# Optimization experiments

Measured on AMD Instinct MI355X. Metric: run time of the kernel, lower is better.

## Reference

```python
import jax, jax.numpy as jnp
import numpy as np

B, S, E, H, NQ, FF = 4, 1024, 256, 32, 8, 1024
DK = E // H  # 8, equals n_wires of the quantum attention layer
EPS = 1e-5


def layernorm(x, g, b):
    mu = jnp.mean(x, axis=-1, keepdims=True)
    var = jnp.mean(jnp.square(x - mu), axis=-1, keepdims=True)
    return (x - mu) * jax.lax.rsqrt(var + EPS) * g + b


def setup_inputs() -> dict:
    key = jax.random.key(0)
    ks = jax.random.split(key, 20)
    s = lambda n: 1.0 / np.sqrt(n)
    return {
        "x": jax.random.normal(ks[0], (B, S, E), dtype=jnp.float32),
        # quantum attention trainable RX angles (one per wire)
        "theta_attn": jax.random.uniform(ks[1], (DK,), minval=-np.pi, maxval=np.pi),
        # nn.MultiheadAttention packed in-proj and out-proj
        "w_in": jax.random.normal(ks[2], (3 * E, E)) * s(E),
        "b_in": jnp.zeros((3 * E,), jnp.float32),
        "w_out": jax.random.normal(ks[3], (E, E)) * s(E),
        "b_out": jnp.zeros((E,), jnp.float32),
        # combine linear
        "w_comb": jax.random.normal(ks[4], (E, E)) * s(E),
        "b_comb": jnp.zeros((E,), jnp.float32),
        # layernorms
        "g1": jnp.ones((E,), jnp.float32), "be1": jnp.zeros((E,), jnp.float32),
        "g2": jnp.ones((E,), jnp.float32), "be2": jnp.zeros((E,), jnp.float32),
        # FFN: input_proj, quantum RY angles, linear1, linear2
        "w_ip": jax.random.normal(ks[5], (NQ, E)) * s(E),
        "b_ip": jnp.zeros((NQ,), jnp.float32),
        "theta_ffn": jax.random.uniform(ks[6], (NQ,), minval=-np.pi, maxval=np.pi),
        "w1": jax.random.normal(ks[7], (FF, NQ)) * s(NQ),
        "b1": jnp.zeros((FF,), jnp.float32),
        "w2": jax.random.normal(ks[8], (E, FF)) * s(FF),
        "b2": jnp.zeros((E,), jnp.float32),
    }


def reference(x, theta_attn, w_in, b_in, w_out, b_out, w_comb, b_comb,
              g1, be1, g2, be2, w_ip, b_ip, theta_ffn, w1, b1, w2, b2):
    batch, seq, embed = x.shape
    # ---- QuantumAttention ----
    # per-head RX(x_i) encoding followed by trainable RX(theta_i): <Z_i> = cos(x_i + theta_i)
    xh = x.reshape(batch, seq, H, DK)            # [B,S,H,dk]
    q_out = jnp.cos(xh + theta_attn).reshape(batch, seq, embed)
    # standard multi-head self-attention on q_out (q=k=v)
    qkv = q_out @ w_in.T + b_in                  # [B,S,3E]
    q, k, v = jnp.split(qkv, 3, axis=-1)
    def heads(t):
        return t.reshape(batch, seq, H, DK).transpose(0, 2, 1, 3)  # [B,H,S,dk]
    q, k, v = heads(q), heads(k), heads(v)
    scores = jnp.einsum('bhqd,bhkd->bhqk', q, k) / np.sqrt(DK)
    attn = jax.nn.softmax(scores, axis=-1)
    ctx = jnp.einsum('bhqk,bhkd->bhqd', attn, v)
    ctx = ctx.transpose(0, 2, 1, 3).reshape(batch, seq, embed)
    attn_out = (ctx @ w_out.T + b_out) @ w_comb.T + b_comb
    # ---- residual + norm1 ----
    h = layernorm(x + attn_out, g1, be1)
    # ---- QuantumFeedForward ----
    proj = h @ w_ip.T + b_ip                     # [B,S,NQ]
    # RX(x) encoding then trainable RY(phi): <Z> = cos(phi) * cos(x)
    qf = jnp.cos(theta_ffn) * jnp.cos(proj)
    ffn_out = jax.nn.relu(qf @ w1.T + b1) @ w2.T + b2
    # ---- residual + norm2 ----
    return layernorm(h + ffn_out, g2, be2)
```

## Files before the change

kernel.cpp:

```cpp
#include <hip/hip_runtime.h>
#include <hip/hip_bf16.h>

#define B_  4
#define S_  1024
#define E_  256
#define H_  32
#define NQ_ 8
#define FF_ 1024
#define M_  (B_*S_)
#define QS  0.5100880289202462f
#define VSTRIDE 1036

typedef __attribute__((ext_vector_type(8))) short bf16x8;
typedef __attribute__((ext_vector_type(4))) short short4v;
typedef __attribute__((ext_vector_type(4))) float f32x4;

#if __has_builtin(__builtin_amdgcn_exp2f)
#define EXP2 __builtin_amdgcn_exp2f
#else
#define EXP2 exp2f
#endif

__device__ inline short f2bf(float f) {
    union { float f; unsigned u; } v; v.f = f;
    unsigned r = (v.u + 0x7fff + ((v.u >> 16) & 1)) >> 16;
    return (short)r;
}

__device__ inline float bf2f(ushort u_) {
    union { unsigned u; float f; } c; c.u = ((unsigned)u_) << 16; return c.f;
}

__device__ inline unsigned pk2(float a, float b) {
    __hip_bfloat162 h = __float22bfloat162_rn(make_float2(a, b));
    union { __hip_bfloat162 h; unsigned u; } c; c.h = h;
    return c.u;
}

__global__ __launch_bounds__(256) void d1_kernel(
        const float* __restrict__ x, const float* __restrict__ theta_attn,
        const float* __restrict__ w_in, const float* __restrict__ b_in,
        const float* __restrict__ w_out, const float* __restrict__ w_comb,
        const float* __restrict__ b_out, const float* __restrict__ b_comb,
        const float* __restrict__ w2,
        ushort* __restrict__ qkv_bf, ushort* __restrict__ weff_bf,
        float* __restrict__ beff, ushort* __restrict__ w2_bf) {
    __shared__ ushort As[128 * 64];
    __shared__ ushort Bs[64 * 64];
    __shared__ float red[4];
    int bid = blockIdx.x, tid = threadIdx.x;

    if (bid >= 392) {
        if (bid < 648) {
            int i = bid - 392;
            float p = w_comb[(size_t)i * 256 + tid] * b_out[tid];
#pragma unroll
            for (int o = 32; o > 0; o >>= 1) p += __shfl_xor(p, o);
            if ((tid & 63) == 0) red[tid >> 6] = p;
            __syncthreads();
            if (tid == 0) beff[i] = red[0] + red[1] + red[2] + red[3] + b_comb[i];
        } else {
            int i = (bid - 648) * 256 + tid;
            float4 v = ((const float4*)w2)[i];
            short4v o = {f2bf(v.x), f2bf(v.y), f2bf(v.z), f2bf(v.w)};
            ((short4v*)w2_bf)[i] = o;
        }
        return;
    }

    bool isW = bid >= 384;
    int bm, bn;
    if (!isW) { bm = (bid / 12) * 128; bn = (bid % 12) * 64; }
    else      { int t = bid - 384; bm = (t >> 2) * 128; bn = (t & 3) * 64; }

    int w = tid >> 6, l = tid & 63, lq = l & 15, hi = l >> 4;
    int wm = w & 1, wn = w >> 1;
    f32x4 acc[4][2] = {};
    int srow = tid >> 3;
    int sk = (tid & 7) * 8;
    float wscale = isW ? 1.f : ((bn < 256) ? QS : 1.f);
    float th[8];
    if (!isW) {
#pragma unroll
        for (int j = 0; j < 8; ++j) th[j] = theta_attn[j];
    }

    for (int k0 = 0; k0 < 256; k0 += 64) {
        __syncthreads();
        if (!isW) {
#pragma unroll
            for (int it = 0; it < 4; ++it) {
                int row = it * 32 + srow;
                const float* xp = x + (size_t)(bm + row) * 256 + k0 + sk;
                float4 a = *(const float4*)xp;
                float4 b = *(const float4*)(xp + 4);
                bf16x8 o;
                o[0] = f2bf(__cosf(a.x + th[0]));
                o[1] = f2bf(__cosf(a.y + th[1]));
                o[2] = f2bf(__cosf(a.z + th[2]));
                o[3] = f2bf(__cosf(a.w + th[3]));
                o[4] = f2bf(__cosf(b.x + th[4]));
                o[5] = f2bf(__cosf(b.y + th[5]));
                o[6] = f2bf(__cosf(b.z + th[6]));
                o[7] = f2bf(__cosf(b.w + th[7]));
                *(bf16x8*)((char*)As + row * 128 + ((sk * 2) ^ ((row & 7) << 4))) = o;
            }
#pragma unroll
            for (int it = 0; it < 2; ++it) {
                int row = it * 32 + srow;
                const float* wp = w_in + (size_t)(bn + row) * 256 + k0 + sk;
                float4 a = *(const float4*)wp;
                float4 b = *(const float4*)(wp + 4);
                bf16x8 o;
                o[0] = f2bf(a.x * wscale); o[1] = f2bf(a.y * wscale);
                o[2] = f2bf(a.z * wscale); o[3] = f2bf(a.w * wscale);
                o[4] = f2bf(b.x * wscale); o[5] = f2bf(b.y * wscale);
                o[6] = f2bf(b.z * wscale); o[7] = f2bf(b.w * wscale);
                *(bf16x8*)((char*)Bs + row * 128 + ((sk * 2) ^ ((row & 7) << 4))) = o;
            }
        } else {
#pragma unroll
            for (int it = 0; it < 4; ++it) {
                int row = it * 32 + srow;
                const float* wp = w_comb + (size_t)(bm + row) * 256 + k0 + sk;
                float4 a = *(const float4*)wp;
                float4 b = *(const float4*)(wp + 4);
                bf16x8 o;
                o[0] = f2bf(a.x); o[1] = f2bf(a.y); o[2] = f2bf(a.z); o[3] = f2bf(a.w);
                o[4] = f2bf(b.x); o[5] = f2bf(b.y); o[6] = f2bf(b.z); o[7] = f2bf(b.w);
                *(bf16x8*)((char*)As + row * 128 + ((sk * 2) ^ ((row & 7) << 4))) = o;
            }
            int nl = tid & 63, kg = tid >> 6;
#pragma unroll
            for (int kk = 0; kk < 16; ++kk) {
                int kb = (kg * 16 + kk) * 2;
                float v = w_out[(size_t)(k0 + kg * 16 + kk) * 256 + bn + nl];
                *(ushort*)((char*)Bs + nl * 128 + (kb ^ ((nl & 7) << 4))) = (ushort)f2bf(v);
            }
        }
        __syncthreads();
#pragma unroll
        for (int kk = 0; kk < 2; ++kk) {
            bf16x8 af[4], bfr[2];
#pragma unroll
            for (int mf = 0; mf < 4; ++mf) {
                int row = wm * 64 + mf * 16 + lq;
                af[mf] = *(const bf16x8*)((const char*)As + row * 128 +
                                          ((kk * 64 + hi * 16) ^ ((row & 7) << 4)));
            }
#pragma unroll
            for (int nf = 0; nf < 2; ++nf) {
                int row = wn * 32 + nf * 16 + lq;
                bfr[nf] = *(const bf16x8*)((const char*)Bs + row * 128 +
                                           ((kk * 64 + hi * 16) ^ ((row & 7) << 4)));
            }
#pragma unroll
            for (int mf = 0; mf < 4; ++mf)
#pragma unroll
                for (int nf = 0; nf < 2; ++nf)
                    acc[mf][nf] = __builtin_amdgcn_mfma_f32_16x16x32_bf16(af[mf], bfr[nf], acc[mf][nf], 0, 0, 0);
        }
    }
    ushort* Cp = isW ? weff_bf : qkv_bf;
    int Nd = isW ? 256 : 768;
#pragma unroll
    for (int mf = 0; mf < 4; ++mf)
#pragma unroll
        for (int nf = 0; nf < 2; ++nf) {
            int n = bn + wn * 32 + nf * 16 + lq;
            float bv = isW ? 0.f : b_in[n] * wscale;
#pragma unroll
            for (int r = 0; r < 4; ++r) {
                int m = bm + wm * 64 + mf * 16 + hi * 4 + r;
                Cp[(size_t)m * Nd + n] = (ushort)f2bf(acc[mf][nf][r] + bv);
            }
        }
}

__global__ __launch_bounds__(256, 4) void attn_mfma_kernel(const ushort* __restrict__ qkv,
                                                           ushort* __restrict__ ctx) {
    __shared__ ushort ks[S_ * 8];
    __shared__ ushort vt[9 * VSTRIDE + 4];
    int qt = blockIdx.x, h = blockIdx.y, b = blockIdx.z;
    int tid = threadIdx.x;
    const ushort* base = qkv + (size_t)b * S_ * (3 * E_) + h * 8;

    for (int i = tid; i < S_; i += 256) {
        const ushort* rp = base + (size_t)i * (3 * E_);
        bf16x8 kv = *(const bf16x8*)(rp + E_);
        bf16x8 vv = *(const bf16x8*)(rp + 2 * E_);
        *(bf16x8*)&ks[i * 8] = kv;
        int kf = (i >> 4) & 3, hh = (i >> 2) & 3, s = i & 3;
        int pv = (i & ~63) + ((kf >> 1) << 5) + (hh << 3) + ((kf & 1) << 2) + s;
#pragma unroll
        for (int d = 0; d < 8; ++d) vt[d * VSTRIDE + pv] = vv[d];
        vt[8 * VSTRIDE + pv] = 0x3F80;
    }
    __syncthreads();

    int w = tid >> 6, l = tid & 63, lq = l & 15, g = l >> 4;

    bf16x8 qfrag[2];
#pragma unroll
    for (int qf = 0; qf < 2; ++qf) {
        bf16x8 qv = {};
        if (g == 0)
            qv = *(const bf16x8*)(base + (size_t)(qt * 128 + w * 32 + qf * 16 + lq) * (3 * E_));
        qfrag[qf] = qv;
    }

    f32x4 ctxa[2] = {{0.f,0.f,0.f,0.f},{0.f,0.f,0.f,0.f}};
    const f32x4 zf = {0.f, 0.f, 0.f, 0.f};

    for (int kt = 0; kt < 16; ++kt) {
        bf16x8 kfrag[4];
#pragma unroll
        for (int kf = 0; kf < 4; ++kf) {
            bf16x8 kv = {};
            if (g == 0) kv = *(bf16x8*)&ks[(kt * 64 + kf * 16 + lq) * 8];
            kfrag[kf] = kv;
        }
        bf16x8 vf0 = *(bf16x8*)&vt[lq * VSTRIDE + kt * 64 + g * 8];
        bf16x8 vf1 = *(bf16x8*)&vt[lq * VSTRIDE + kt * 64 + 32 + g * 8];
#pragma unroll
        for (int qf = 0; qf < 2; ++qf) {
            f32x4 st[4];
#pragma unroll
            for (int kf = 0; kf < 4; ++kf)
                st[kf] = __builtin_amdgcn_mfma_f32_16x16x32_bf16(kfrag[kf], qfrag[qf], zf, 0, 0, 0);
            union { unsigned u[4]; bf16x8 v; } p0, p1;
            p0.u[0] = pk2(EXP2(st[0][0]), EXP2(st[0][1]));
            p0.u[1] = pk2(EXP2(st[0][2]), EXP2(st[0][3]));
            p0.u[2] = pk2(EXP2(st[1][0]), EXP2(st[1][1]));
            p0.u[3] = pk2(EXP2(st[1][2]), EXP2(st[1][3]));
            p1.u[0] = pk2(EXP2(st[2][0]), EXP2(st[2][1]));
            p1.u[1] = pk2(EXP2(st[2][2]), EXP2(st[2][3]));
            p1.u[2] = pk2(EXP2(st[3][0]), EXP2(st[3][1]));
            p1.u[3] = pk2(EXP2(st[3][2]), EXP2(st[3][3]));
            ctxa[qf] = __builtin_amdgcn_mfma_f32_16x16x32_bf16(p0.v, vf0, ctxa[qf], 0, 0, 0);
            ctxa[qf] = __builtin_amdgcn_mfma_f32_16x16x32_bf16(p1.v, vf1, ctxa[qf], 0, 0, 0);
        }
    }

#pragma unroll
    for (int qf = 0; qf < 2; ++qf) {
        int src = (l & 48) + 8;
        float s0 = __shfl(ctxa[qf][0], src);
        float s1 = __shfl(ctxa[qf][1], src);
        float s2 = __shfl(ctxa[qf][2], src);
        float s3 = __shfl(ctxa[qf][3], src);
        if (lq < 8) {
            int tok = b * S_ + qt * 128 + w * 32 + qf * 16 + g * 4;
            ushort* cp = ctx + (size_t)tok * E_ + h * 8 + lq;
            cp[0]      = (ushort)f2bf(ctxa[qf][0] / s0);
            cp[E_]     = (ushort)f2bf(ctxa[qf][1] / s1);
            cp[2 * E_] = (ushort)f2bf(ctxa[qf][2] / s2);
            cp[3 * E_] = (ushort)f2bf(ctxa[qf][3] / s3);
        }
    }
}

__global__ __launch_bounds__(256) void d3_kernel(
        const ushort* __restrict__ ctx, const ushort* __restrict__ weff,
        const float* __restrict__ beff, const float* __restrict__ x,
        const float* __restrict__ g1, const float* __restrict__ be1,
        const float* __restrict__ w_ip, const float* __restrict__ b_ip,
        const float* __restrict__ theta_ffn,
        float* __restrict__ h, float* __restrict__ qf) {
    __shared__ union {
        struct { ushort As[16 * 64]; ushort Bs[256 * 64]; } st;
        ushort hl[16 * 264];
    } u;
    __shared__ float red[2][16][4];
    int tid = threadIdx.x;
    int bm = blockIdx.x * 16;
    int wn = tid >> 6, l = tid & 63, lq = l & 15, hi = l >> 4;
    f32x4 acc[4] = {};

    for (int k0 = 0; k0 < 256; k0 += 64) {
        __syncthreads();
        if (tid < 128) {
            int row = tid >> 3, sk = (tid & 7) * 8;
            bf16x8 v = *(const bf16x8*)(ctx + (size_t)(bm + row) * 256 + k0 + sk);
            *(bf16x8*)((char*)u.st.As + row * 128 + ((sk * 2) ^ ((row & 7) << 4))) = v;
        }
#pragma unroll
        for (int it = 0; it < 8; ++it) {
            int v8 = it * 256 + tid;
            int row = v8 >> 3, kb = (v8 & 7) * 16;
            bf16x8 v = *(const bf16x8*)(weff + (size_t)row * 256 + k0 + (kb >> 1));
            *(bf16x8*)((char*)u.st.Bs + row * 128 + (kb ^ ((row & 7) << 4))) = v;
        }
        __syncthreads();
#pragma unroll
        for (int kk = 0; kk < 2; ++kk) {
            bf16x8 af, bfr[4];
            af = *(const bf16x8*)((const char*)u.st.As + lq * 128 +
                                  ((kk * 64 + hi * 16) ^ ((lq & 7) << 4)));
#pragma unroll
            for (int nf = 0; nf < 4; ++nf) {
                int row = wn * 64 + nf * 16 + lq;
                bfr[nf] = *(const bf16x8*)((const char*)u.st.Bs + row * 128 +
                                           ((kk * 64 + hi * 16) ^ ((row & 7) << 4)));
            }
#pragma unroll
            for (int nf = 0; nf < 4; ++nf)
                acc[nf] = __builtin_amdgcn_mfma_f32_16x16x32_bf16(af, bfr[nf], acc[nf], 0, 0, 0);
        }
    }
    __syncthreads();

    float vv[4][4];
    float rs[4] = {}, rq[4] = {};
#pragma unroll
    for (int nf = 0; nf < 4; ++nf) {
        int n = wn * 64 + nf * 16 + lq;
        float bv = beff[n];
#pragma unroll
        for (int r = 0; r < 4; ++r) {
            int m = bm + hi * 4 + r;
            float val = acc[nf][r] + bv + x[(size_t)m * 256 + n];
            vv[nf][r] = val;
            rs[r] += val;
            rq[r] += val * val;
        }
    }
#pragma unroll
    for (int o = 1; o < 16; o <<= 1)
#pragma unroll
        for (int r = 0; r < 4; ++r) {
            rs[r] += __shfl_xor(rs[r], o);
            rq[r] += __shfl_xor(rq[r], o);
        }
    if (lq == 0) {
#pragma unroll
        for (int r = 0; r < 4; ++r) {
            red[0][hi * 4 + r][wn] = rs[r];
            red[1][hi * 4 + r][wn] = rq[r];
        }
    }
    __syncthreads();
#pragma unroll
    for (int r = 0; r < 4; ++r) {
        int row = hi * 4 + r;
        float st_ = red[0][row][0] + red[0][row][1] + red[0][row][2] + red[0][row][3];
        float sq_ = red[1][row][0] + red[1][row][1] + red[1][row][2] + red[1][row][3];
        float mu = st_ * (1.f / 256.f);
        float var = sq_ * (1.f / 256.f) - mu * mu;
        rs[r] = mu;
        rq[r] = rsqrtf(var + 1e-5f);
    }
    __syncthreads();
#pragma unroll
    for (int nf = 0; nf < 4; ++nf) {
        int n = wn * 64 + nf * 16 + lq;
        float gn = g1[n], bn_ = be1[n];
#pragma unroll
        for (int r = 0; r < 4; ++r) {
            int row = hi * 4 + r;
            float vn = (vv[nf][r] - rs[r]) * rq[r] * gn + bn_;
            h[(size_t)(bm + row) * 256 + n] = vn;
            u.hl[row * 264 + n] = (ushort)f2bf(vn);
        }
    }
    __syncthreads();

    if (tid < 128) {
        int tok = tid >> 3, wq = tid & 7;
        const float* wip = w_ip + wq * 256;
        float pr = 0.f;
#pragma unroll
        for (int c = 0; c < 32; ++c) {
            bf16x8 hv = *(const bf16x8*)&u.hl[tok * 264 + c * 8];
            float4 wa = *(const float4*)(wip + c * 8);
            float4 wb = *(const float4*)(wip + c * 8 + 4);
            pr += bf2f((ushort)hv[0]) * wa.x + bf2f((ushort)hv[1]) * wa.y
                + bf2f((ushort)hv[2]) * wa.z + bf2f((ushort)hv[3]) * wa.w
                + bf2f((ushort)hv[4]) * wb.x + bf2f((ushort)hv[5]) * wb.y
                + bf2f((ushort)hv[6]) * wb.z + bf2f((ushort)hv[7]) * wb.w;
        }
        qf[(size_t)(bm + tok) * NQ_ + wq] = __cosf(theta_ffn[wq]) * __cosf(pr + b_ip[wq]);
    }
}

__global__ __launch_bounds__(256) void d4_kernel(
        const float* __restrict__ qf, const float* __restrict__ w1,
        const float* __restrict__ b1, const ushort* __restrict__ w2b,
        const float* __restrict__ b2, const float* __restrict__ h,
        const float* __restrict__ g2, const float* __restrict__ be2,
        float* __restrict__ out) {
    __shared__ ushort As[16 * 64];
    __shared__ ushort Bs[256 * 64];
    __shared__ ushort w1l[FF_ * 8];
    __shared__ float b1l[FF_];
    __shared__ float qfl[16 * 8];
    __shared__ float red[2][16][4];
    int tid = threadIdx.x;
    int bm = blockIdx.x * 16;
    int wn = tid >> 6, l = tid & 63, lq = l & 15, hi = l >> 4;
    f32x4 acc[4] = {};

#pragma unroll
    for (int it = 0; it < 32; ++it) w1l[it * 256 + tid] = (ushort)f2bf(w1[it * 256 + tid]);
#pragma unroll
    for (int it = 0; it < 4; ++it) b1l[it * 256 + tid] = b1[it * 256 + tid];
    if (tid < 128) qfl[tid] = qf[(size_t)bm * NQ_ + tid];
    __syncthreads();

    for (int k0 = 0; k0 < 1024; k0 += 64) {
        __syncthreads();
        if (tid < 128) {
            int row = tid >> 3, j8 = tid & 7;
            int f0 = k0 + j8 * 8;
            float q[8];
#pragma unroll
            for (int k = 0; k < 8; ++k) q[k] = qfl[row * 8 + k];
            bf16x8 o;
#pragma unroll
            for (int j = 0; j < 8; ++j) {
                bf16x8 wv = *(const bf16x8*)&w1l[(f0 + j) * 8];
                float s = b1l[f0 + j];
#pragma unroll
                for (int k = 0; k < 8; ++k) s += q[k] * bf2f((ushort)wv[k]);
                o[j] = f2bf(fmaxf(s, 0.f));
            }
            int sk = j8 * 8;
            *(bf16x8*)((char*)As + row * 128 + ((sk * 2) ^ ((row & 7) << 4))) = o;
        }
#pragma unroll
        for (int it = 0; it < 8; ++it) {
            int v8 = it * 256 + tid;
            int row = v8 >> 3, kb = (v8 & 7) * 16;
            bf16x8 v = *(const bf16x8*)(w2b + (size_t)row * 1024 + k0 + (kb >> 1));
            *(bf16x8*)((char*)Bs + row * 128 + (kb ^ ((row & 7) << 4))) = v;
        }
        __syncthreads();
#pragma unroll
        for (int kk = 0; kk < 2; ++kk) {
            bf16x8 af, bfr[4];
            af = *(const bf16x8*)((const char*)As + lq * 128 +
                                  ((kk * 64 + hi * 16) ^ ((lq & 7) << 4)));
#pragma unroll
            for (int nf = 0; nf < 4; ++nf) {
                int row = wn * 64 + nf * 16 + lq;
                bfr[nf] = *(const bf16x8*)((const char*)Bs + row * 128 +
                                           ((kk * 64 + hi * 16) ^ ((row & 7) << 4)));
            }
#pragma unroll
            for (int nf = 0; nf < 4; ++nf)
                acc[nf] = __builtin_amdgcn_mfma_f32_16x16x32_bf16(af, bfr[nf], acc[nf], 0, 0, 0);
        }
    }

    float vv[4][4];
    float rs[4] = {}, rq[4] = {};
#pragma unroll
    for (int nf = 0; nf < 4; ++nf) {
        int n = wn * 64 + nf * 16 + lq;
        float bv = b2[n];
#pragma unroll
        for (int r = 0; r < 4; ++r) {
            int m = bm + hi * 4 + r;
            float val = acc[nf][r] + bv + h[(size_t)m * 256 + n];
            vv[nf][r] = val;
            rs[r] += val;
            rq[r] += val * val;
        }
    }
#pragma unroll
    for (int o = 1; o < 16; o <<= 1)
#pragma unroll
        for (int r = 0; r < 4; ++r) {
            rs[r] += __shfl_xor(rs[r], o);
            rq[r] += __shfl_xor(rq[r], o);
        }
    if (lq == 0) {
#pragma unroll
        for (int r = 0; r < 4; ++r) {
            red[0][hi * 4 + r][wn] = rs[r];
            red[1][hi * 4 + r][wn] = rq[r];
        }
    }
    __syncthreads();
#pragma unroll
    for (int r = 0; r < 4; ++r) {
        int row = hi * 4 + r;
        float st_ = red[0][row][0] + red[0][row][1] + red[0][row][2] + red[0][row][3];
        float sq_ = red[1][row][0] + red[1][row][1] + red[1][row][2] + red[1][row][3];
        float mu = st_ * (1.f / 256.f);
        float var = sq_ * (1.f / 256.f) - mu * mu;
        rs[r] = mu;
        rq[r] = rsqrtf(var + 1e-5f);
    }
#pragma unroll
    for (int nf = 0; nf < 4; ++nf) {
        int n = wn * 64 + nf * 16 + lq;
        float gn = g2[n], bn_ = be2[n];
#pragma unroll
        for (int r = 0; r < 4; ++r) {
            int row = hi * 4 + r;
            out[(size_t)(bm + row) * 256 + n] =
                (vv[nf][r] - rs[r]) * rq[r] * gn + bn_;
        }
    }
}

extern "C" void kernel_launch(void* const* d_in, const int* in_sizes, int n_in,
                              void* d_out, int out_size, void* d_ws, size_t ws_size,
                              hipStream_t stream) {
    const float* x          = (const float*)d_in[0];
    const float* theta_attn = (const float*)d_in[1];
    const float* w_in       = (const float*)d_in[2];
    const float* b_in       = (const float*)d_in[3];
    const float* w_out      = (const float*)d_in[4];
    const float* b_out      = (const float*)d_in[5];
    const float* w_comb     = (const float*)d_in[6];
    const float* b_comb     = (const float*)d_in[7];
    const float* g1         = (const float*)d_in[8];
    const float* be1        = (const float*)d_in[9];
    const float* g2         = (const float*)d_in[10];
    const float* be2        = (const float*)d_in[11];
    const float* w_ip       = (const float*)d_in[12];
    const float* b_ip       = (const float*)d_in[13];
    const float* theta_ffn  = (const float*)d_in[14];
    const float* w1         = (const float*)d_in[15];
    const float* b1         = (const float*)d_in[16];
    const float* w2         = (const float*)d_in[17];
    const float* b2         = (const float*)d_in[18];
    float* out = (float*)d_out;

    char* wsb = (char*)d_ws;
    ushort* qkv_bf  = (ushort*)(wsb);
    ushort* ctx_bf  = (ushort*)(wsb + (6u << 20));
    float*  h       = (float*)(wsb + (8u << 20));
    float*  qf      = (float*)(wsb + (12u << 20));
    ushort* weff_bf = (ushort*)(wsb + (13u << 20));
    ushort* w2_bf   = (ushort*)(wsb + (13u << 20) + 131072);
    float*  beff    = (float*)(wsb + (14u << 20));

    d1_kernel<<<904, 256, 0, stream>>>(x, theta_attn, w_in, b_in, w_out, w_comb,
                                       b_out, b_comb, w2, qkv_bf, weff_bf, beff, w2_bf);
    attn_mfma_kernel<<<dim3(S_ / 128, H_, B_), 256, 0, stream>>>(qkv_bf, ctx_bf);
    d3_kernel<<<M_ / 16, 256, 0, stream>>>(ctx_bf, weff_bf, beff, x, g1, be1,
                                           w_ip, b_ip, theta_ffn, h, qf);
    d4_kernel<<<M_ / 16, 256, 0, stream>>>(qf, w1, b1, w2_bf, b2, h, g2, be2, out);
}
```

Baseline: 183.0 us.

## Fuse norm1/FFN kernels and read GEMM operands directly from global

Merges the d3 and d4 kernels into one, so h and qf stay in shared memory instead of round-tripping through global workspace, and removes one launch. The FFN hidden activations (relu(qf@w1^T+b1)) are computed once into a full 16x1024 LDS tile, and both GEMMs now load weight fragments straight from global/L2 instead of staging them through LDS with barriers. The attention inner loop also raises wave priority around the MFMA/exp section. In exchange, LDS use per block grows and the uncoalesced direct global fragment loads may lose bandwidth efficiency. The FFN projection now uses fp32 h instead of bf16.

Result: no change. 183.0 us (-0.0%).

```diff
diff --git a/kernel.cpp b/kernel.cpp
--- a/kernel.cpp
+++ b/kernel.cpp
@@ -222,6 +222,7 @@
         }
         bf16x8 vf0 = *(bf16x8*)&vt[lq * VSTRIDE + kt * 64 + g * 8];
         bf16x8 vf1 = *(bf16x8*)&vt[lq * VSTRIDE + kt * 64 + 32 + g * 8];
+        __builtin_amdgcn_s_setprio(1);
 #pragma unroll
         for (int qf = 0; qf < 2; ++qf) {
             f32x4 st[4];
@@ -240,6 +241,7 @@
             ctxa[qf] = __builtin_amdgcn_mfma_f32_16x16x32_bf16(p0.v, vf0, ctxa[qf], 0, 0, 0);
             ctxa[qf] = __builtin_amdgcn_mfma_f32_16x16x32_bf16(p1.v, vf1, ctxa[qf], 0, 0, 0);
         }
+        __builtin_amdgcn_s_setprio(0);
     }
 
 #pragma unroll
@@ -260,55 +262,38 @@
     }
 }
 
-__global__ __launch_bounds__(256) void d3_kernel(
+__global__ __launch_bounds__(256) void d34_kernel(
         const ushort* __restrict__ ctx, const ushort* __restrict__ weff,
         const float* __restrict__ beff, const float* __restrict__ x,
         const float* __restrict__ g1, const float* __restrict__ be1,
         const float* __restrict__ w_ip, const float* __restrict__ b_ip,
         const float* __restrict__ theta_ffn,
-        float* __restrict__ h, float* __restrict__ qf) {
-    __shared__ union {
-        struct { ushort As[16 * 64]; ushort Bs[256 * 64]; } st;
-        ushort hl[16 * 264];
-    } u;
+        const float* __restrict__ w1, const float* __restrict__ b1,
+        const ushort* __restrict__ w2b, const float* __restrict__ b2,
+        const float* __restrict__ g2, const float* __restrict__ be2,
+        float* __restrict__ out) {
+    __shared__ float hs[16 * 260];
+    __shared__ float qfl[16 * 8];
+    __shared__ ushort ts[16 * 1024];
     __shared__ float red[2][16][4];
     int tid = threadIdx.x;
     int bm = blockIdx.x * 16;
     int wn = tid >> 6, l = tid & 63, lq = l & 15, hi = l >> 4;
+
     f32x4 acc[4] = {};
-
+#pragma unroll
     for (int k0 = 0; k0 < 256; k0 += 64) {
-        __syncthreads();
-        if (tid < 128) {
-            int row = tid >> 3, sk = (tid & 7) * 8;
-            bf16x8 v = *(const bf16x8*)(ctx + (size_t)(bm + row) * 256 + k0 + sk);
-            *(bf16x8*)((char*)u.st.As + row * 128 + ((sk * 2) ^ ((row & 7) << 4))) = v;
-        }
-#pragma unroll
-        for (int it = 0; it < 8; ++it) {
-            int v8 = it * 256 + tid;
-            int row = v8 >> 3, kb = (v8 & 7) * 16;
-            bf16x8 v = *(const bf16x8*)(weff + (size_t)row * 256 + k0 + (kb >> 1));
-            *(bf16x8*)((char*)u.st.Bs + row * 128 + (kb ^ ((row & 7) << 4))) = v;
-        }
-        __syncthreads();
 #pragma unroll
         for (int kk = 0; kk < 2; ++kk) {
-            bf16x8 af, bfr[4];
-            af = *(const bf16x8*)((const char*)u.st.As + lq * 128 +
-                                  ((kk * 64 + hi * 16) ^ ((lq & 7) << 4)));
+            bf16x8 af = *(const bf16x8*)(ctx + (size_t)(bm + lq) * 256 + k0 + kk * 32 + hi * 8);
 #pragma unroll
             for (int nf = 0; nf < 4; ++nf) {
-                int row = wn * 64 + nf * 16 + lq;
-                bfr[nf] = *(const bf16x8*)((const char*)u.st.Bs + row * 128 +
-                                           ((kk * 64 + hi * 16) ^ ((row & 7) << 4)));
-            }
-#pragma unroll
-            for (int nf = 0; nf < 4; ++nf)
-                acc[nf] = __builtin_amdgcn_mfma_f32_16x16x32_bf16(af, bfr[nf], acc[nf], 0, 0, 0);
-        }
-    }
-    __syncthreads();
+                int rb = wn * 64 + nf * 16 + lq;
+                bf16x8 bf_ = *(const bf16x8*)(weff + (size_t)rb * 256 + k0 + kk * 32 + hi * 8);
+                acc[nf] = __builtin_amdgcn_mfma_f32_16x16x32_bf16(af, bf_, acc[nf], 0, 0, 0);
+            }
+        }
+    }
 
     float vv[4][4];
     float rs[4] = {}, rq[4] = {};
@@ -350,7 +335,6 @@
         rs[r] = mu;
         rq[r] = rsqrtf(var + 1e-5f);
     }
-    __syncthreads();
 #pragma unroll
     for (int nf = 0; nf < 4; ++nf) {
         int n = wn * 64 + nf * 16 + lq;
@@ -358,9 +342,7 @@
 #pragma unroll
         for (int r = 0; r < 4; ++r) {
             int row = hi * 4 + r;
-            float vn = (vv[nf][r] - rs[r]) * rq[r] * gn + bn_;
-            h[(size_t)(bm + row) * 256 + n] = vn;
-            u.hl[row * 264 + n] = (ushort)f2bf(vn);
+            hs[row * 260 + n] = (vv[nf][r] - rs[r]) * rq[r] * gn + bn_;
         }
     }
     __syncthreads();
@@ -370,115 +352,82 @@
         const float* wip = w_ip + wq * 256;
         float pr = 0.f;
 #pragma unroll
-        for (int c = 0; c < 32; ++c) {
-            bf16x8 hv = *(const bf16x8*)&u.hl[tok * 264 + c * 8];
-            float4 wa = *(const float4*)(wip + c * 8);
-            float4 wb = *(const float4*)(wip + c * 8 + 4);
-            pr += bf2f((ushort)hv[0]) * wa.x + bf2f((ushort)hv[1]) * wa.y
-                + bf2f((ushort)hv[2]) * wa.z + bf2f((ushort)hv[3]) * wa.w
-                + bf2f((ushort)hv[4]) * wb.x + bf2f((ushort)hv[5]) * wb.y
-                + bf2f((ushort)hv[6]) * wb.z + bf2f((ushort)hv[7]) * wb.w;
-        }
-        qf[(size_t)(bm + tok) * NQ_ + wq] = __cosf(theta_ffn[wq]) * __cosf(pr + b_ip[wq]);
-    }
-}
-
-__global__ __launch_bounds__(256) void d4_kernel(
-        const float* __restrict__ qf, const float* __restrict__ w1,
-        const float* __restrict__ b1, const ushort* __restrict__ w2b,
-        const float* __restrict__ b2, const float* __restrict__ h,
-        const float* __restrict__ g2, const float* __restrict__ be2,
-        float* __restrict__ out) {
-    __shared__ ushort As[16 * 64];
-    __shared__ ushort Bs[256 * 64];
-    __shared__ ushort w1l[FF_ * 8];
-    __shared__ float b1l[FF_];
-    __shared__ float qfl[16 * 8];
-    __shared__ float red[2][16][4];
-    int tid = threadIdx.x;
-    int bm = blockIdx.x * 16;
-    int wn = tid >> 6, l = tid & 63, lq = l & 15, hi = l >> 4;
-    f32x4 acc[4] = {};
-
-#pragma unroll
-    for (int it = 0; it < 32; ++it) w1l[it * 256 + tid] = (ushort)f2bf(w1[it * 256 + tid]);
-#pragma unroll
-    for (int it = 0; it < 4; ++it) b1l[it * 256 + tid] = b1[it * 256 + tid];
-    if (tid < 128) qfl[tid] = qf[(size_t)bm * NQ_ + tid];
-    __syncthreads();
-
+        for (int c = 0; c < 64; ++c) {
+            float4 hv = *(const float4*)&hs[tok * 260 + c * 4];
+            float4 wv = *(const float4*)(wip + c * 4);
+            pr += hv.x * wv.x + hv.y * wv.y + hv.z * wv.z + hv.w * wv.w;
+        }
+        qfl[tok * 8 + wq] = __cosf(theta_ffn[wq]) * __cosf(pr + b_ip[wq]);
+    }
+    __syncthreads();
+
+    {
+        int row = tid & 15, fb = tid >> 4;
+        float q[8];
+#pragma unroll
+        for (int k = 0; k < 8; ++k) q[k] = qfl[row * 8 + k];
+#pragma unroll
+        for (int j8 = 0; j8 < 8; ++j8) {
+            int f0 = fb * 64 + j8 * 8;
+            bf16x8 o;
+#pragma unroll
+            for (int j = 0; j < 8; ++j) {
+                const float* wp = w1 + (size_t)(f0 + j) * 8;
+                float4 wa = *(const float4*)wp;
+                float4 wb = *(const float4*)(wp + 4);
+                float s = b1[f0 + j]
+                        + q[0] * wa.x + q[1] * wa.y + q[2] * wa.z + q[3] * wa.w
+                        + q[4] * wb.x + q[5] * wb.y + q[6] * wb.z + q[7] * wb.w;
+                o[j] = f2bf(fmaxf(s, 0.f));
+            }
+            *(bf16x8*)((char*)ts + row * 2048 + ((f0 * 2) ^ ((row & 7) << 4))) = o;
+        }
+    }
+    __syncthreads();
+
+    f32x4 acc2[4] = {};
+#pragma unroll 4
     for (int k0 = 0; k0 < 1024; k0 += 64) {
-        __syncthreads();
-        if (tid < 128) {
-            int row = tid >> 3, j8 = tid & 7;
-            int f0 = k0 + j8 * 8;
-            float q[8];
-#pragma unroll
-            for (int k = 0; k < 8; ++k) q[k] = qfl[row * 8 + k];
-            bf16x8 o;
-#pragma unroll
-            for (int j = 0; j < 8; ++j) {
-                bf16x8 wv = *(const bf16x8*)&w1l[(f0 + j) * 8];
-                float s = b1l[f0 + j];
-#pragma unroll
-                for (int k = 0; k < 8; ++k) s += q[k] * bf2f((ushort)wv[k]);
-                o[j] = f2bf(fmaxf(s, 0.f));
-            }
-            int sk = j8 * 8;
-            *(bf16x8*)((char*)As + row * 128 + ((sk * 2) ^ ((row & 7) << 4))) = o;
-        }
-#pragma unroll
-        for (int it = 0; it < 8; ++it) {
-            int v8 = it * 256 + tid;
-            int row = v8 >> 3, kb = (v8 & 7) * 16;
-            bf16x8 v = *(const bf16x8*)(w2b + (size_t)row * 1024 + k0 + (kb >> 1));
-            *(bf16x8*)((char*)Bs + row * 128 + (kb ^ ((row & 7) << 4))) = v;
-        }
-        __syncthreads();
 #pragma unroll
         for (int kk = 0; kk < 2; ++kk) {
-            bf16x8 af, bfr[4];
-            af = *(const bf16x8*)((const char*)As + lq * 128 +
-                                  ((kk * 64 + hi * 16) ^ ((lq & 7) << 4)));
+            bf16x8 af = *(const bf16x8*)((const char*)ts + lq * 2048 +
+                                         ((k0 * 2 + kk * 64 + hi * 16) ^ ((lq & 7) << 4)));
 #pragma unroll
             for (int nf = 0; nf < 4; ++nf) {
-                int row = wn * 64 + nf * 16 + lq;
-                bfr[nf] = *(const bf16x8*)((const char*)Bs + row * 128 +
-                                           ((kk * 64 + hi * 16) ^ ((row & 7) << 4)));
-            }
-#pragma unroll
-            for (int nf = 0; nf < 4; ++nf)
-                acc[nf] = __builtin_amdgcn_mfma_f32_16x16x32_bf16(af, bfr[nf], acc[nf], 0, 0, 0);
-        }
-    }
-
-    float vv[4][4];
-    float rs[4] = {}, rq[4] = {};
+                int rb = wn * 64 + nf * 16 + lq;
+                bf16x8 bf_ = *(const bf16x8*)(w2b + (size_t)rb * 1024 + k0 + kk * 32 + hi * 8);
+                acc2[nf] = __builtin_amdgcn_mfma_f32_16x16x32_bf16(af, bf_, acc2[nf], 0, 0, 0);
+            }
+        }
+    }
+
+    float rs2[4] = {}, rq2[4] = {};
 #pragma unroll
     for (int nf = 0; nf < 4; ++nf) {
         int n = wn * 64 + nf * 16 + lq;
         float bv = b2[n];
 #pragma unroll
         for (int r = 0; r < 4; ++r) {
-            int m = bm + hi * 4 + r;
-            float val = acc[nf][r] + bv + h[(size_t)m * 256 + n];
+            int row = hi * 4 + r;
+            float val = acc2[nf][r] + bv + hs[row * 260 + n];
             vv[nf][r] = val;
-            rs[r] += val;
-            rq[r] += val * val;
+            rs2[r] += val;
+            rq2[r] += val * val;
         }
     }
 #pragma unroll
     for (int o = 1; o < 16; o <<= 1)
 #pragma unroll
         for (int r = 0; r < 4; ++r) {
-            rs[r] += __shfl_xor(rs[r], o);
-            rq[r] += __shfl_xor(rq[r], o);
-        }
+            rs2[r] += __shfl_xor(rs2[r], o);
+            rq2[r] += __shfl_xor(rq2[r], o);
+        }
+    __syncthreads();
     if (lq == 0) {
 #pragma unroll
         for (int r = 0; r < 4; ++r) {
-            red[0][hi * 4 + r][wn] = rs[r];
-            red[1][hi * 4 + r][wn] = rq[r];
+            red[0][hi * 4 + r][wn] = rs2[r];
+            red[1][hi * 4 + r][wn] = rq2[r];
         }
     }
     __syncthreads();
@@ -489,8 +438,8 @@
         float sq_ = red[1][row][0] + red[1][row][1] + red[1][row][2] + red[1][row][3];
         float mu = st_ * (1.f / 256.f);
         float var = sq_ * (1.f / 256.f) - mu * mu;
-        rs[r] = mu;
-        rq[r] = rsqrtf(var + 1e-5f);
+        rs2[r] = mu;
+        rq2[r] = rsqrtf(var + 1e-5f);
     }
 #pragma unroll
     for (int nf = 0; nf < 4; ++nf) {
@@ -500,7 +449,7 @@
         for (int r = 0; r < 4; ++r) {
             int row = hi * 4 + r;
             out[(size_t)(bm + row) * 256 + n] =
-                (vv[nf][r] - rs[r]) * rq[r] * gn + bn_;
+                (vv[nf][r] - rs2[r]) * rq2[r] * gn + bn_;
         }
     }
 }
@@ -532,16 +481,14 @@
     char* wsb = (char*)d_ws;
     ushort* qkv_bf  = (ushort*)(wsb);
     ushort* ctx_bf  = (ushort*)(wsb + (6u << 20));
-    float*  h       = (float*)(wsb + (8u << 20));
-    float*  qf      = (float*)(wsb + (12u << 20));
-    ushort* weff_bf = (ushort*)(wsb + (13u << 20));
-    ushort* w2_bf   = (ushort*)(wsb + (13u << 20) + 131072);
-    float*  beff    = (float*)(wsb + (14u << 20));
+    ushort* weff_bf = (ushort*)(wsb + (8u << 20));
+    ushort* w2_bf   = (ushort*)(wsb + (8u << 20) + 131072);
+    float*  beff    = (float*)(wsb + (9u << 20));
 
     d1_kernel<<<904, 256, 0, stream>>>(x, theta_attn, w_in, b_in, w_out, w_comb,
                                        b_out, b_comb, w2, qkv_bf, weff_bf, beff, w2_bf);
     attn_mfma_kernel<<<dim3(S_ / 128, H_, B_), 256, 0, stream>>>(qkv_bf, ctx_bf);
-    d3_kernel<<<M_ / 16, 256, 0, stream>>>(ctx_bf, weff_bf, beff, x, g1, be1,
-                                           w_ip, b_ip, theta_ffn, h, qf);
-    d4_kernel<<<M_ / 16, 256, 0, stream>>>(qf, w1, b1, w2_bf, b2, h, g2, be2, out);
-}
+    d34_kernel<<<M_ / 16, 256, 0, stream>>>(ctx_bf, weff_bf, beff, x, g1, be1,
+                                            w_ip, b_ip, theta_ffn, w1, b1,
+                                            w2_bf, b2, g2, be2, out);
+}
```
